# Performance work log

Measured on AMD Instinct MI355X. Metric: run time of the kernel, lower is better.

The kernel has to match this reference:

```python
import jax, jax.numpy as jnp
import numpy as np

DIM = 1024
HEADS = 16
HEAD_DIM = DIM // HEADS
RPE_K = 16
B, T = 4, 1024


def setup_inputs() -> dict:
    key = jax.random.key(0)
    ks = jax.random.split(key, 12)
    s = 1.0 / np.sqrt(DIM)
    inp = {
        'q': jax.random.normal(ks[0], (B, T, DIM), jnp.float32),
        'k': jax.random.normal(ks[1], (B, T, DIM), jnp.float32),
        'v': jax.random.normal(ks[2], (B, T, DIM), jnp.float32),
        'Wq': jax.random.normal(ks[3], (DIM, DIM), jnp.float32) * s,
        'bq': jnp.zeros((DIM,), jnp.float32),
        'Wk': jax.random.normal(ks[4], (DIM, DIM), jnp.float32) * s,
        'bk': jnp.zeros((DIM,), jnp.float32),
        'Wv': jax.random.normal(ks[5], (DIM, DIM), jnp.float32) * s,
        'bv': jnp.zeros((DIM,), jnp.float32),
        'rpe_w': jax.random.normal(ks[6], (2 * RPE_K + 1, 2 * HEAD_DIM), jnp.float32) * 0.02,
        'Wo': jax.random.normal(ks[7], (DIM, DIM), jnp.float32) * s,
        'bo': jnp.zeros((DIM,), jnp.float32),
    }
    return inp


def reference(q, k, v, Wq, bq, Wk, bk, Wv, bv, rpe_w, Wo, bo):
    b, ql = q.shape[:2]
    kl = k.shape[1]
    split = lambda x: x.reshape(b, -1, HEADS, HEAD_DIM).transpose(0, 2, 1, 3)  # b h t d
    qh = split(q @ Wq.T + bq)
    kh = split(k @ Wk.T + bk)
    vh = split(v @ Wv.T + bv)
    # note: original scales q BEFORE both the k-dot and the rpe_q einsum
    qh = qh / np.sqrt(HEAD_DIM)
    # relative distance table (constant ints)
    idx = jnp.arange(max(ql, kl))
    dist = jnp.clip(idx[:, None] - idx[None, :], -RPE_K, RPE_K) + RPE_K
    dist = dist[:ql, :kl]
    rpe = rpe_w[dist]                      # (ql, kl, 2*HEAD_DIM)
    rpe_q, rpe_v = jnp.split(rpe, 2, axis=-1)
    energy = jnp.einsum('bhqd,bhkd->bhqk', qh, kh)
    energy = energy + jnp.einsum('bhqd,qkd->bhqk', qh, rpe_q)
    alignment = jax.nn.softmax(energy, axis=-1)
    context = jnp.einsum('bhqk,bhkd->bhqd', alignment, vh)
    context = context + jnp.einsum('bhqk,qkd->bhqd', alignment, rpe_v)
    context = context.transpose(0, 2, 1, 3).reshape(b, ql, DIM)
    out = context @ Wo.T + bo
    return (out, alignment)
```

## Files before the change

### kernel.cpp

```cpp
#include <hip/hip_runtime.h>
#include <stdint.h>

typedef unsigned short u16;
typedef unsigned int   u32;
typedef short bf16x8 __attribute__((ext_vector_type(8)));
typedef float floatx4 __attribute__((ext_vector_type(4)));

#define OFF_XQ   0u
#define OFF_XK   4194304u
#define OFF_XV   8388608u
#define OFF_WQ   12582912u
#define OFF_WK   13631488u
#define OFF_WV   14680064u
#define OFF_WO   15728640u
#define OFF_QH   16777216u
#define OFF_KH   20971520u
#define OFF_VT   25165824u
#define OFF_CTX  29360128u

__device__ __forceinline__ u16 f2b(float f){
  u32 u = __float_as_uint(f);
  u = (u + 0x7fffu + ((u >> 16) & 1u)) >> 16;
  return (u16)u;
}
__device__ __forceinline__ float b2f(u16 h){
  return __uint_as_float(((u32)h) << 16);
}

__global__ __launch_bounds__(256) void convert_kernel(
    const float* __restrict__ q, const float* __restrict__ k, const float* __restrict__ v,
    const float* __restrict__ Wq, const float* __restrict__ Wk, const float* __restrict__ Wv,
    const float* __restrict__ Wo, u16* __restrict__ ws){
  int y = blockIdx.y;
  const float* src; u16* dst; int n;
  switch(y){
    case 0: src=q;  dst=ws+OFF_XQ; n=4194304; break;
    case 1: src=k;  dst=ws+OFF_XK; n=4194304; break;
    case 2: src=v;  dst=ws+OFF_XV; n=4194304; break;
    case 3: src=Wq; dst=ws+OFF_WQ; n=1048576; break;
    case 4: src=Wk; dst=ws+OFF_WK; n=1048576; break;
    case 5: src=Wv; dst=ws+OFF_WV; n=1048576; break;
    default:src=Wo; dst=ws+OFF_WO; n=1048576; break;
  }
  int idx = (blockIdx.x*256 + threadIdx.x)*4;
  if (idx >= n) return;
  float4 f = *(const float4*)(src + idx);
  ushort4 o;
  o.x = f2b(f.x); o.y = f2b(f.y); o.z = f2b(f.z); o.w = f2b(f.w);
  *(ushort4*)(dst + idx) = o;
}

template<int MODE>
__global__ __launch_bounds__(256) void gemm_kernel(
    const u16* __restrict__ A0, const u16* __restrict__ B0,
    const float* __restrict__ b0, const float* __restrict__ b1, const float* __restrict__ b2,
    u16* __restrict__ ws, float* __restrict__ outF){
  __shared__ u16 As[128][40];
  __shared__ u16 Bs[128][40];
  int z = (MODE==0) ? blockIdx.z : 0;
  const u16* A  = A0 + (size_t)z*4194304u;
  const u16* Bm = B0 + (size_t)z*1048576u;
  const float* bias = (MODE==0) ? (z==0?b0:(z==1?b1:b2)) : b0;
  int tid  = threadIdx.x;
  int lane = tid & 63, wave = tid >> 6;
  int wm = (wave>>1)*64, wn = (wave&1)*64;
  int m_base = blockIdx.y*128, n_base = blockIdx.x*128;
  floatx4 acc[4][4] = {};
  int fr = lane & 15, fo = (lane>>4)*8;
  for (int kb = 0; kb < 1024; kb += 32){
    #pragma unroll
    for (int p=0;p<2;p++){
      int L = tid + p*256;
      int row = L>>2, seg = (L&3)*8;
      *(uint4*)(&As[row][seg]) = *(const uint4*)(A  + (size_t)(m_base+row)*1024 + kb + seg);
      *(uint4*)(&Bs[row][seg]) = *(const uint4*)(Bm + (size_t)(n_base+row)*1024 + kb + seg);
    }
    __syncthreads();
    bf16x8 af[4], bfr[4];
    #pragma unroll
    for (int i=0;i<4;i++){
      af[i]  = *(const bf16x8*)(&As[wm + i*16 + fr][fo]);
      bfr[i] = *(const bf16x8*)(&Bs[wn + i*16 + fr][fo]);
    }
    #pragma unroll
    for (int i=0;i<4;i++)
      #pragma unroll
      for (int j=0;j<4;j++)
        acc[i][j] = __builtin_amdgcn_mfma_f32_16x16x32_bf16(af[i], bfr[j], acc[i][j], 0,0,0);
    __syncthreads();
  }
  int col = lane & 15, rb = (lane>>4)*4;
  #pragma unroll
  for (int i=0;i<4;i++){
    #pragma unroll
    for (int j=0;j<4;j++){
      int nn = n_base + wn + j*16 + col;
      float bv = bias[nn];
      #pragma unroll
      for (int r=0;r<4;r++){
        int mm = m_base + wm + i*16 + rb + r;
        float v = acc[i][j][r] + bv;
        if (MODE==0){
          if (z==0) v *= 0.125f;
          int b = mm>>10, t = mm&1023, h = nn>>6, d = nn&63;
          u32 base = (z==0)?OFF_QH:((z==1)?OFF_KH:OFF_VT);
          u32 idx = ((u32)(b*16+h))<<16;
          idx += (z==2) ? ((u32)(d<<10)+(u32)t) : ((u32)(t<<6)+(u32)d);
          ws[base + idx] = f2b(v);
        } else {
          outF[(size_t)mm*1024 + nn] = v;
        }
      }
    }
  }
}

__global__ __launch_bounds__(256) void attn_kernel(
    const u16* __restrict__ ws, const float* __restrict__ rpe_w,
    float* __restrict__ d_out, u16* __restrict__ ctx){
  __shared__ u16   P[16][1032];
  __shared__ u16   qs[16][64];
  __shared__ float proj[16][33];
  __shared__ float rpev[33][64];
  __shared__ float sacc[16][3];
  __shared__ float slds[16][33];
  __shared__ float linv[16];

  int bid = blockIdx.x;
  int qt = bid & 63, bh = bid >> 6;
  int q0 = qt * 16;
  int tid = threadIdx.x, lane = tid & 63, wave = tid >> 6;

  const u16* qh = ws + OFF_QH + (size_t)bh*65536;
  const u16* kh = ws + OFF_KH + (size_t)bh*65536;
  const u16* vT = ws + OFF_VT + (size_t)bh*65536;

  if (tid < 128){
    int r = tid >> 3, c = (tid & 7)*8;
    *(uint4*)(&qs[r][c]) = *(const uint4*)(qh + (size_t)(q0+r)*64 + c);
  }
  for (int i = tid; i < 33*64; i += 256){
    int t = i >> 6, d = i & 63;
    rpev[t][d] = rpe_w[t*128 + 64 + d];
  }
  if (tid < 48) ((float*)sacc)[tid] = 0.f;
  __syncthreads();

  for (int i = tid; i < 16*33; i += 256){
    int r = i / 33, t = i - r*33;
    float s = 0.f;
    #pragma unroll
    for (int d=0; d<64; d++) s += b2f(qs[r][d]) * rpe_w[t*128 + d];
    proj[r][t] = s;
  }
  __syncthreads();

  int col = lane & 15, rb = (lane>>4)*4, fo = (lane>>4)*8;
  bf16x8 aq0 = *(const bf16x8*)(&qs[col][fo]);
  bf16x8 aq1 = *(const bf16x8*)(&qs[col][32 + fo]);

  float tot[4] = {0,0,0,0}, lo[4] = {0,0,0,0}, hi[4] = {0,0,0,0};
  for (int kb = 0; kb < 1024; kb += 64){
    int key = kb + wave*16 + col;
    const u16* kp = kh + (size_t)key*64 + fo;
    bf16x8 bk0 = *(const bf16x8*)(kp);
    bf16x8 bk1 = *(const bf16x8*)(kp + 32);
    floatx4 s4 = {0.f,0.f,0.f,0.f};
    s4 = __builtin_amdgcn_mfma_f32_16x16x32_bf16(aq0, bk0, s4, 0,0,0);
    s4 = __builtin_amdgcn_mfma_f32_16x16x32_bf16(aq1, bk1, s4, 0,0,0);
    #pragma unroll
    for (int r=0;r<4;r++){
      int row = rb + r;
      int qg = q0 + row;
      int dd = qg - key;
      int bkt = min(max(dd, -16), 16) + 16;
      float p = __expf(s4[r] + proj[row][bkt]);
      P[row][key] = f2b(p);
      tot[r] += p;
      if      (key <= qg - 16) lo[r] += p;
      else if (key >= qg + 16) hi[r] += p;
    }
  }
  #pragma unroll
  for (int r=0;r<4;r++){
    #pragma unroll
    for (int m=8;m>=1;m>>=1){
      tot[r] += __shfl_xor(tot[r], m, 16);
      lo[r]  += __shfl_xor(lo[r],  m, 16);
      hi[r]  += __shfl_xor(hi[r],  m, 16);
    }
  }
  if (col == 0){
    #pragma unroll
    for (int r=0;r<4;r++){
      atomicAdd(&sacc[rb+r][0], tot[r]);
      atomicAdd(&sacc[rb+r][1], lo[r]);
      atomicAdd(&sacc[rb+r][2], hi[r]);
    }
  }
  __syncthreads();

  if (tid < 16){
    linv[tid] = 1.f / sacc[tid][0];
    slds[tid][32] = sacc[tid][1];
    slds[tid][0]  = sacc[tid][2];
  }
  for (int i = tid; i < 16*31; i += 256){
    int r = i / 31, t = 1 + (i - r*31);
    int kk = q0 + r + 16 - t;
    slds[r][t] = (kk >= 0 && kk < 1024) ? b2f(P[r][kk]) : 0.f;
  }
  __syncthreads();

  {
    int row = tid >> 4, c0 = (tid & 15)*4;
    float li = linv[row];
    float* outA = d_out + 4194304u + ((size_t)(bh*1024 + q0 + row))*1024;
    #pragma unroll
    for (int i=0;i<16;i++){
      int kcol = c0 + i*64;
      ushort4 pv = *(const ushort4*)(&P[row][kcol]);
      float4 o;
      o.x = b2f(pv.x)*li; o.y = b2f(pv.y)*li;
      o.z = b2f(pv.z)*li; o.w = b2f(pv.w)*li;
      *(float4*)(outA + kcol) = o;
    }
  }

  floatx4 o4 = {0.f,0.f,0.f,0.f};
  int n0 = wave*16;
  {
    const u16* vbase = vT + (size_t)(n0 + col)*1024;
    for (int kk = 0; kk < 1024; kk += 32){
      bf16x8 ap  = *(const bf16x8*)(&P[col][kk + fo]);
      bf16x8 bv8 = *(const bf16x8*)(vbase + kk + fo);
      o4 = __builtin_amdgcn_mfma_f32_16x16x32_bf16(ap, bv8, o4, 0,0,0);
    }
  }
  {
    int b = bh >> 4, h = bh & 15;
    #pragma unroll
    for (int r=0;r<4;r++){
      int row = rb + r;
      int d = n0 + col;
      float sv = 0.f;
      #pragma unroll
      for (int t=0;t<33;t++) sv += slds[row][t]*rpev[t][d];
      float v = (o4[r] + sv) * linv[row];
      ctx[((size_t)(b*1024 + q0 + row))*1024 + h*64 + d] = f2b(v);
    }
  }
}

extern "C" void kernel_launch(void* const* d_in, const int* in_sizes, int n_in,
                              void* d_out, int out_size, void* d_ws, size_t ws_size,
                              hipStream_t stream){
  const float* q  = (const float*)d_in[0];
  const float* k  = (const float*)d_in[1];
  const float* v  = (const float*)d_in[2];
  const float* Wq = (const float*)d_in[3];
  const float* bq = (const float*)d_in[4];
  const float* Wk = (const float*)d_in[5];
  const float* bk = (const float*)d_in[6];
  const float* Wv = (const float*)d_in[7];
  const float* bv = (const float*)d_in[8];
  const float* rpe= (const float*)d_in[9];
  const float* Wo = (const float*)d_in[10];
  const float* bo = (const float*)d_in[11];
  u16* ws = (u16*)d_ws;
  float* out = (float*)d_out;

  convert_kernel<<<dim3(4096,7), 256, 0, stream>>>(q,k,v,Wq,Wk,Wv,Wo, ws);
  gemm_kernel<0><<<dim3(8,32,3), 256, 0, stream>>>(ws+OFF_XQ, ws+OFF_WQ, bq, bk, bv, ws, nullptr);
  attn_kernel<<<dim3(4096), 256, 0, stream>>>(ws, rpe, out, ws+OFF_CTX);
  gemm_kernel<1><<<dim3(8,32), 256, 0, stream>>>(ws+OFF_CTX, ws+OFF_WO, bo, nullptr, nullptr, ws, out);
}
```

Baseline: 603.5 us.

## Fuse bf16 conversion into GEMM loads and restructure attention to keep P in registers

Removes the separate fp32-to-bf16 conversion kernel: the GEMMs now read fp32 activations and weights directly and pack them to bf16 while staging into shared memory. The V projection writes its transposed output through a shared-memory transpose so global stores are coalesced. The attention kernel computes the q·rpe projection with MFMA, keeps the unnormalized probabilities packed in registers instead of a 32KB shared P tile, and streams them through a small double-buffered LDS chunk for the PV matmul. This cuts shared-memory footprint to raise occupancy, at the cost of more register pressure and re-reading the alignment output from global memory for the near-diagonal rpe terms.

```diff
diff --git a/kernel.cpp b/kernel.cpp
--- a/kernel.cpp
+++ b/kernel.cpp
@@ -6,17 +6,11 @@
 typedef short bf16x8 __attribute__((ext_vector_type(8)));
 typedef float floatx4 __attribute__((ext_vector_type(4)));
 
-#define OFF_XQ   0u
-#define OFF_XK   4194304u
-#define OFF_XV   8388608u
-#define OFF_WQ   12582912u
-#define OFF_WK   13631488u
-#define OFF_WV   14680064u
-#define OFF_WO   15728640u
-#define OFF_QH   16777216u
-#define OFF_KH   20971520u
-#define OFF_VT   25165824u
-#define OFF_CTX  29360128u
+#define OFF_QH  0u
+#define OFF_KH  4194304u
+#define OFF_VT  8388608u
+#define OFF_CTX 12582912u
+#define OFF_RPE 16777216u
 
 __device__ __forceinline__ u16 f2b(float f){
   u32 u = __float_as_uint(f);
@@ -26,61 +20,63 @@
 __device__ __forceinline__ float b2f(u16 h){
   return __uint_as_float(((u32)h) << 16);
 }
-
-__global__ __launch_bounds__(256) void convert_kernel(
-    const float* __restrict__ q, const float* __restrict__ k, const float* __restrict__ v,
-    const float* __restrict__ Wq, const float* __restrict__ Wk, const float* __restrict__ Wv,
-    const float* __restrict__ Wo, u16* __restrict__ ws){
-  int y = blockIdx.y;
-  const float* src; u16* dst; int n;
-  switch(y){
-    case 0: src=q;  dst=ws+OFF_XQ; n=4194304; break;
-    case 1: src=k;  dst=ws+OFF_XK; n=4194304; break;
-    case 2: src=v;  dst=ws+OFF_XV; n=4194304; break;
-    case 3: src=Wq; dst=ws+OFF_WQ; n=1048576; break;
-    case 4: src=Wk; dst=ws+OFF_WK; n=1048576; break;
-    case 5: src=Wv; dst=ws+OFF_WV; n=1048576; break;
-    default:src=Wo; dst=ws+OFF_WO; n=1048576; break;
-  }
-  int idx = (blockIdx.x*256 + threadIdx.x)*4;
-  if (idx >= n) return;
-  float4 f = *(const float4*)(src + idx);
-  ushort4 o;
-  o.x = f2b(f.x); o.y = f2b(f.y); o.z = f2b(f.z); o.w = f2b(f.w);
-  *(ushort4*)(dst + idx) = o;
+__device__ __forceinline__ u32 pack2(float a, float b){
+  return (u32)f2b(a) | ((u32)f2b(b) << 16);
+}
+
+__global__ __launch_bounds__(256) void rpe_kernel(const float* __restrict__ rpe, u16* __restrict__ ws){
+  int idx = blockIdx.x*256 + threadIdx.x;
+  if (idx >= 6144) return;
+  ws[OFF_RPE + idx] = (idx < 4224) ? f2b(rpe[idx]) : (u16)0;
 }
 
 template<int MODE>
 __global__ __launch_bounds__(256) void gemm_kernel(
-    const u16* __restrict__ A0, const u16* __restrict__ B0,
+    const float* __restrict__ A0f, const float* __restrict__ A1f, const float* __restrict__ A2f,
+    const u16*  __restrict__ Abf,
+    const float* __restrict__ B0f, const float* __restrict__ B1f, const float* __restrict__ B2f,
     const float* __restrict__ b0, const float* __restrict__ b1, const float* __restrict__ b2,
-    u16* __restrict__ ws, float* __restrict__ outF){
-  __shared__ u16 As[128][40];
-  __shared__ u16 Bs[128][40];
+    u16* __restrict__ ws, float* __restrict__ outF)
+{
+  __shared__ u16 smem[(MODE==0) ? 18432 : 10240];
+  u16* As = smem;
+  u16* Bs = smem + 5120;
   int z = (MODE==0) ? blockIdx.z : 0;
-  const u16* A  = A0 + (size_t)z*4194304u;
-  const u16* Bm = B0 + (size_t)z*1048576u;
+  const float* Af = (MODE==0) ? (z==0?A0f:(z==1?A1f:A2f)) : nullptr;
+  const float* Bf = (MODE==0) ? (z==0?B0f:(z==1?B1f:B2f)) : B0f;
   const float* bias = (MODE==0) ? (z==0?b0:(z==1?b1:b2)) : b0;
+
   int tid  = threadIdx.x;
   int lane = tid & 63, wave = tid >> 6;
   int wm = (wave>>1)*64, wn = (wave&1)*64;
   int m_base = blockIdx.y*128, n_base = blockIdx.x*128;
   floatx4 acc[4][4] = {};
   int fr = lane & 15, fo = (lane>>4)*8;
+
   for (int kb = 0; kb < 1024; kb += 32){
     #pragma unroll
     for (int p=0;p<2;p++){
       int L = tid + p*256;
       int row = L>>2, seg = (L&3)*8;
-      *(uint4*)(&As[row][seg]) = *(const uint4*)(A  + (size_t)(m_base+row)*1024 + kb + seg);
-      *(uint4*)(&Bs[row][seg]) = *(const uint4*)(Bm + (size_t)(n_base+row)*1024 + kb + seg);
+      if (MODE==0){
+        const float* ap = Af + (size_t)(m_base+row)*1024 + kb + seg;
+        float4 a0 = *(const float4*)ap; float4 a1 = *(const float4*)(ap+4);
+        uint4 av = { pack2(a0.x,a0.y), pack2(a0.z,a0.w), pack2(a1.x,a1.y), pack2(a1.z,a1.w) };
+        *(uint4*)(&As[row*40+seg]) = av;
+      } else {
+        *(uint4*)(&As[row*40+seg]) = *(const uint4*)(Abf + (size_t)(m_base+row)*1024 + kb + seg);
+      }
+      const float* bp = Bf + (size_t)(n_base+row)*1024 + kb + seg;
+      float4 c0 = *(const float4*)bp; float4 c1 = *(const float4*)(bp+4);
+      uint4 bv = { pack2(c0.x,c0.y), pack2(c0.z,c0.w), pack2(c1.x,c1.y), pack2(c1.z,c1.w) };
+      *(uint4*)(&Bs[row*40+seg]) = bv;
     }
     __syncthreads();
     bf16x8 af[4], bfr[4];
     #pragma unroll
     for (int i=0;i<4;i++){
-      af[i]  = *(const bf16x8*)(&As[wm + i*16 + fr][fo]);
-      bfr[i] = *(const bf16x8*)(&Bs[wn + i*16 + fr][fo]);
+      af[i]  = *(const bf16x8*)(&As[(wm + i*16 + fr)*40 + fo]);
+      bfr[i] = *(const bf16x8*)(&Bs[(wn + i*16 + fr)*40 + fo]);
     }
     #pragma unroll
     for (int i=0;i<4;i++)
@@ -89,7 +85,31 @@
         acc[i][j] = __builtin_amdgcn_mfma_f32_16x16x32_bf16(af[i], bfr[j], acc[i][j], 0,0,0);
     __syncthreads();
   }
+
   int col = lane & 15, rb = (lane>>4)*4;
+  if (MODE==0 && z==2){
+    u16* Tr = smem + wave*4608;
+    #pragma unroll
+    for (int j=0;j<4;j++){
+      float bv = bias[n_base + wn + j*16 + col];
+      #pragma unroll
+      for (int i=0;i<4;i++){
+        #pragma unroll
+        for (int r=0;r<4;r++)
+          Tr[(j*16+col)*72 + (i*16+rb+r)] = f2b(acc[i][j][r] + bv);
+      }
+    }
+    __syncthreads();
+    int b = (m_base+wm)>>10, t0 = (m_base+wm)&1023;
+    int n = n_base + wn + lane; int h = n>>6, d = n&63;
+    u16* dst = ws + OFF_VT + (size_t)(b*16+h)*65536 + (size_t)d*1024 + t0;
+    const u16* src = smem + wave*4608 + lane*72;
+    #pragma unroll
+    for (int mm=0;mm<64;mm+=8)
+      *(uint4*)(dst+mm) = *(const uint4*)(src+mm);
+    return;
+  }
+
   #pragma unroll
   for (int i=0;i<4;i++){
     #pragma unroll
@@ -103,10 +123,8 @@
         if (MODE==0){
           if (z==0) v *= 0.125f;
           int b = mm>>10, t = mm&1023, h = nn>>6, d = nn&63;
-          u32 base = (z==0)?OFF_QH:((z==1)?OFF_KH:OFF_VT);
-          u32 idx = ((u32)(b*16+h))<<16;
-          idx += (z==2) ? ((u32)(d<<10)+(u32)t) : ((u32)(t<<6)+(u32)d);
-          ws[base + idx] = f2b(v);
+          u32 base = (z==0)?OFF_QH:OFF_KH;
+          ws[base + (((u32)(b*16+h))<<16) + (u32)(t*64+d)] = f2b(v);
         } else {
           outF[(size_t)mm*1024 + nn] = v;
         }
@@ -117,138 +135,142 @@
 
 __global__ __launch_bounds__(256) void attn_kernel(
     const u16* __restrict__ ws, const float* __restrict__ rpe_w,
-    float* __restrict__ d_out, u16* __restrict__ ctx){
-  __shared__ u16   P[16][1032];
-  __shared__ u16   qs[16][64];
-  __shared__ float proj[16][33];
-  __shared__ float rpev[33][64];
-  __shared__ float sacc[16][3];
-  __shared__ float slds[16][33];
-  __shared__ float linv[16];
+    float* __restrict__ d_out, u16* __restrict__ ctx)
+{
+  __shared__ float proj[16*49];
+  __shared__ float slds[16*33];
+  __shared__ float sacc[4*16*3];
+  __shared__ float linvS[16];
+  __shared__ u16   Pc[2][16*72];
 
   int bid = blockIdx.x;
   int qt = bid & 63, bh = bid >> 6;
   int q0 = qt * 16;
   int tid = threadIdx.x, lane = tid & 63, wave = tid >> 6;
+  int col = lane & 15, rb = (lane>>4)*4, fo = (lane>>4)*8;
 
   const u16* qh = ws + OFF_QH + (size_t)bh*65536;
   const u16* kh = ws + OFF_KH + (size_t)bh*65536;
   const u16* vT = ws + OFF_VT + (size_t)bh*65536;
-
-  if (tid < 128){
-    int r = tid >> 3, c = (tid & 7)*8;
-    *(uint4*)(&qs[r][c]) = *(const uint4*)(qh + (size_t)(q0+r)*64 + c);
-  }
-  for (int i = tid; i < 33*64; i += 256){
-    int t = i >> 6, d = i & 63;
-    rpev[t][d] = rpe_w[t*128 + 64 + d];
-  }
-  if (tid < 48) ((float*)sacc)[tid] = 0.f;
-  __syncthreads();
-
-  for (int i = tid; i < 16*33; i += 256){
-    int r = i / 33, t = i - r*33;
-    float s = 0.f;
-    #pragma unroll
-    for (int d=0; d<64; d++) s += b2f(qs[r][d]) * rpe_w[t*128 + d];
-    proj[r][t] = s;
-  }
-  __syncthreads();
-
-  int col = lane & 15, rb = (lane>>4)*4, fo = (lane>>4)*8;
-  bf16x8 aq0 = *(const bf16x8*)(&qs[col][fo]);
-  bf16x8 aq1 = *(const bf16x8*)(&qs[col][32 + fo]);
-
-  float tot[4] = {0,0,0,0}, lo[4] = {0,0,0,0}, hi[4] = {0,0,0,0};
-  for (int kb = 0; kb < 1024; kb += 64){
-    int key = kb + wave*16 + col;
-    const u16* kp = kh + (size_t)key*64 + fo;
-    bf16x8 bk0 = *(const bf16x8*)(kp);
-    bf16x8 bk1 = *(const bf16x8*)(kp + 32);
+  const u16* rpeB = ws + OFF_RPE;
+
+  bf16x8 aq0 = *(const bf16x8*)(qh + (size_t)(q0+col)*64 + fo);
+  bf16x8 aq1 = *(const bf16x8*)(qh + (size_t)(q0+col)*64 + 32 + fo);
+
+  #pragma unroll
+  for (int c=0;c<3;c++){
+    int t = c*16 + col;
+    bf16x8 br0 = *(const bf16x8*)(rpeB + t*128 + fo);
+    bf16x8 br1 = *(const bf16x8*)(rpeB + t*128 + 32 + fo);
+    floatx4 pj = {0.f,0.f,0.f,0.f};
+    pj = __builtin_amdgcn_mfma_f32_16x16x32_bf16(aq0, br0, pj, 0,0,0);
+    pj = __builtin_amdgcn_mfma_f32_16x16x32_bf16(aq1, br1, pj, 0,0,0);
+    #pragma unroll
+    for (int r=0;r<4;r++) proj[(rb+r)*49 + c*16 + col] = pj[r];
+  }
+  __syncthreads();
+
+  int myq = q0 + col;
+  float tot=0.f, lo=0.f, hi=0.f;
+  u32 pk[16][2];
+  #pragma unroll
+  for (int i=0;i<16;i++){
+    const u16* kp = kh + (size_t)(i*64 + wave*16 + col)*64 + fo;
+    bf16x8 ak0 = *(const bf16x8*)(kp);
+    bf16x8 ak1 = *(const bf16x8*)(kp + 32);
     floatx4 s4 = {0.f,0.f,0.f,0.f};
-    s4 = __builtin_amdgcn_mfma_f32_16x16x32_bf16(aq0, bk0, s4, 0,0,0);
-    s4 = __builtin_amdgcn_mfma_f32_16x16x32_bf16(aq1, bk1, s4, 0,0,0);
+    s4 = __builtin_amdgcn_mfma_f32_16x16x32_bf16(ak0, aq0, s4, 0,0,0);
+    s4 = __builtin_amdgcn_mfma_f32_16x16x32_bf16(ak1, aq1, s4, 0,0,0);
+    int key0 = i*64 + wave*16 + rb;
+    float pv[4];
     #pragma unroll
     for (int r=0;r<4;r++){
-      int row = rb + r;
-      int qg = q0 + row;
-      int dd = qg - key;
-      int bkt = min(max(dd, -16), 16) + 16;
-      float p = __expf(s4[r] + proj[row][bkt]);
-      P[row][key] = f2b(p);
-      tot[r] += p;
-      if      (key <= qg - 16) lo[r] += p;
-      else if (key >= qg + 16) hi[r] += p;
-    }
-  }
+      int dd = myq - (key0 + r);
+      int bkt = min(max(dd,-16),16) + 16;
+      float p = __expf(s4[r] + proj[col*49 + bkt]);
+      tot += p;
+      lo += (dd >= 16)  ? p : 0.f;
+      hi += (dd <= -16) ? p : 0.f;
+      pv[r] = p;
+    }
+    pk[i][0] = pack2(pv[0], pv[1]);
+    pk[i][1] = pack2(pv[2], pv[3]);
+  }
+  tot += __shfl_xor(tot,16); tot += __shfl_xor(tot,32);
+  lo  += __shfl_xor(lo, 16); lo  += __shfl_xor(lo, 32);
+  hi  += __shfl_xor(hi, 16); hi  += __shfl_xor(hi, 32);
+  if (lane < 16){
+    sacc[(wave*16+lane)*3+0] = tot;
+    sacc[(wave*16+lane)*3+1] = lo;
+    sacc[(wave*16+lane)*3+2] = hi;
+  }
+  __syncthreads();
+  if (tid < 16){
+    float T=0.f, L=0.f, H=0.f;
+    #pragma unroll
+    for (int w=0;w<4;w++){
+      T += sacc[(w*16+tid)*3+0];
+      L += sacc[(w*16+tid)*3+1];
+      H += sacc[(w*16+tid)*3+2];
+    }
+    float li = 1.f / T;
+    linvS[tid] = li;
+    slds[tid*33 + 0]  = H*li;
+    slds[tid*33 + 32] = L*li;
+  }
+  __syncthreads();
+
+  float li = linvS[col];
+  float* alig = d_out + 4194304u + ((size_t)(bh*1024 + myq))*1024;
+  #pragma unroll
+  for (int i=0;i<16;i++){
+    float4 o = { b2f((u16)(pk[i][0]&0xffffu))*li, b2f((u16)(pk[i][0]>>16))*li,
+                 b2f((u16)(pk[i][1]&0xffffu))*li, b2f((u16)(pk[i][1]>>16))*li };
+    *(float4*)(alig + i*64 + wave*16 + rb) = o;
+  }
+  __syncthreads();
+
+  const float* aligB = d_out + 4194304u + (size_t)bh*1048576u + (size_t)q0*1024;
+  for (int j = tid; j < 496; j += 256){
+    int r = j/31, t = 1 + (j - r*31);
+    int kk = q0 + r + 16 - t;
+    slds[r*33+t] = (kk>=0 && kk<1024) ? aligB[(size_t)r*1024 + kk] : 0.f;
+  }
+
+  floatx4 o4 = {0.f,0.f,0.f,0.f};
+  const u16* vbase = vT + (size_t)(wave*16 + col)*1024;
+  {
+    uint2 w0 = {pk[0][0], pk[0][1]};
+    *(uint2*)(&Pc[0][col*72 + wave*16 + rb]) = w0;
+  }
+  for (int c2=0;c2<16;c2++){
+    __syncthreads();
+    int buf = c2 & 1;
+    bf16x8 ap0 = *(const bf16x8*)(&Pc[buf][col*72 + fo]);
+    bf16x8 ap1 = *(const bf16x8*)(&Pc[buf][col*72 + 32 + fo]);
+    if (c2 < 15){
+      uint2 wn2 = {pk[c2+1][0], pk[c2+1][1]};
+      *(uint2*)(&Pc[buf^1][col*72 + wave*16 + rb]) = wn2;
+    }
+    bf16x8 bv0 = *(const bf16x8*)(vbase + c2*64 + fo);
+    bf16x8 bv1 = *(const bf16x8*)(vbase + c2*64 + 32 + fo);
+    o4 = __builtin_amdgcn_mfma_f32_16x16x32_bf16(ap0, bv0, o4, 0,0,0);
+    o4 = __builtin_amdgcn_mfma_f32_16x16x32_bf16(ap1, bv1, o4, 0,0,0);
+  }
+  __syncthreads();
+
+  int d = wave*16 + col;
+  float rv[33];
+  #pragma unroll
+  for (int t=0;t<33;t++) rv[t] = rpe_w[t*128 + 64 + d];
+  int b = bh >> 4, h = bh & 15;
   #pragma unroll
   for (int r=0;r<4;r++){
-    #pragma unroll
-    for (int m=8;m>=1;m>>=1){
-      tot[r] += __shfl_xor(tot[r], m, 16);
-      lo[r]  += __shfl_xor(lo[r],  m, 16);
-      hi[r]  += __shfl_xor(hi[r],  m, 16);
-    }
-  }
-  if (col == 0){
-    #pragma unroll
-    for (int r=0;r<4;r++){
-      atomicAdd(&sacc[rb+r][0], tot[r]);
-      atomicAdd(&sacc[rb+r][1], lo[r]);
-      atomicAdd(&sacc[rb+r][2], hi[r]);
-    }
-  }
-  __syncthreads();
-
-  if (tid < 16){
-    linv[tid] = 1.f / sacc[tid][0];
-    slds[tid][32] = sacc[tid][1];
-    slds[tid][0]  = sacc[tid][2];
-  }
-  for (int i = tid; i < 16*31; i += 256){
-    int r = i / 31, t = 1 + (i - r*31);
-    int kk = q0 + r + 16 - t;
-    slds[r][t] = (kk >= 0 && kk < 1024) ? b2f(P[r][kk]) : 0.f;
-  }
-  __syncthreads();
-
-  {
-    int row = tid >> 4, c0 = (tid & 15)*4;
-    float li = linv[row];
-    float* outA = d_out + 4194304u + ((size_t)(bh*1024 + q0 + row))*1024;
-    #pragma unroll
-    for (int i=0;i<16;i++){
-      int kcol = c0 + i*64;
-      ushort4 pv = *(const ushort4*)(&P[row][kcol]);
-      float4 o;
-      o.x = b2f(pv.x)*li; o.y = b2f(pv.y)*li;
-      o.z = b2f(pv.z)*li; o.w = b2f(pv.w)*li;
-      *(float4*)(outA + kcol) = o;
-    }
-  }
-
-  floatx4 o4 = {0.f,0.f,0.f,0.f};
-  int n0 = wave*16;
-  {
-    const u16* vbase = vT + (size_t)(n0 + col)*1024;
-    for (int kk = 0; kk < 1024; kk += 32){
-      bf16x8 ap  = *(const bf16x8*)(&P[col][kk + fo]);
-      bf16x8 bv8 = *(const bf16x8*)(vbase + kk + fo);
-      o4 = __builtin_amdgcn_mfma_f32_16x16x32_bf16(ap, bv8, o4, 0,0,0);
-    }
-  }
-  {
-    int b = bh >> 4, h = bh & 15;
-    #pragma unroll
-    for (int r=0;r<4;r++){
-      int row = rb + r;
-      int d = n0 + col;
-      float sv = 0.f;
-      #pragma unroll
-      for (int t=0;t<33;t++) sv += slds[row][t]*rpev[t][d];
-      float v = (o4[r] + sv) * linv[row];
-      ctx[((size_t)(b*1024 + q0 + row))*1024 + h*64 + d] = f2b(v);
-    }
+    float sv = 0.f;
+    #pragma unroll
+    for (int t=0;t<33;t++) sv += slds[(rb+r)*33+t] * rv[t];
+    float vr = o4[r]*linvS[rb+r] + sv;
+    ctx[((size_t)(b*1024 + q0 + rb + r))*1024 + h*64 + d] = f2b(vr);
   }
 }
 
@@ -270,8 +292,8 @@
   u16* ws = (u16*)d_ws;
   float* out = (float*)d_out;
 
-  convert_kernel<<<dim3(4096,7), 256, 0, stream>>>(q,k,v,Wq,Wk,Wv,Wo, ws);
-  gemm_kernel<0><<<dim3(8,32,3), 256, 0, stream>>>(ws+OFF_XQ, ws+OFF_WQ, bq, bk, bv, ws, nullptr);
+  rpe_kernel<<<dim3(24), 256, 0, stream>>>(rpe, ws);
+  gemm_kernel<0><<<dim3(8,32,3), 256, 0, stream>>>(q,k,v, nullptr, Wq,Wk,Wv, bq,bk,bv, ws, nullptr);
   attn_kernel<<<dim3(4096), 256, 0, stream>>>(ws, rpe, out, ws+OFF_CTX);
-  gemm_kernel<1><<<dim3(8,32), 256, 0, stream>>>(ws+OFF_CTX, ws+OFF_WO, bo, nullptr, nullptr, ws, out);
-}
+  gemm_kernel<1><<<dim3(8,32), 256, 0, stream>>>(nullptr,nullptr,nullptr, ws+OFF_CTX, Wo,nullptr,nullptr, bo,nullptr,nullptr, ws, out);
+}
```

Result: no change. 615.0 us (+1.9%).
